# Kernel optimization log

Measured on AMD Instinct MI355X. Metric: run time of the kernel, lower is better.

## Reference

```python
import jax, jax.numpy as jnp
import numpy as np

EPS = 1e-12  # matches torch.nn.functional.normalize eps


def _normalize(v):
    # L2-normalize along last dim, torch-style eps clamp on the norm
    n = jnp.sqrt(jnp.sum(v * v, axis=-1, keepdims=True))
    return v / jnp.maximum(n, EPS)


def _dis_normalized_l2(n1, n2):
    a = _normalize(n1)
    b = _normalize(n2)
    d_minus = jnp.sum((a - b) ** 2, axis=-1)
    d_plus = jnp.sum((a + b) ** 2, axis=-1)
    return jnp.minimum(d_minus, d_plus)


def setup_inputs() -> dict:
    key = jax.random.key(0)
    k1, k2, k3, k4 = jax.random.split(key, 4)
    B, N, M = 8, 4096, 4096
    return {
        "xyz1": jax.random.normal(k1, (B, N, 3), dtype=jnp.float32),
        "xyz2": jax.random.normal(k2, (B, M, 3), dtype=jnp.float32),
        "normal_rebuild": jax.random.normal(k3, (B, N, 3), dtype=jnp.float32),
        "normal_gt": jax.random.normal(k4, (B, M, 3), dtype=jnp.float32),
    }


def reference(xyz1, xyz2, normal_rebuild, normal_gt):
    # Brute-force chamfer: squared pairwise distances [B, N, M]
    sq1 = jnp.sum(xyz1 * xyz1, axis=-1)  # [B, N]
    sq2 = jnp.sum(xyz2 * xyz2, axis=-1)  # [B, M]
    cross = jnp.einsum("bnd,bmd->bnm", xyz1, xyz2)  # [B, N, M]
    D = sq1[:, :, None] + sq2[:, None, :] - 2.0 * cross

    dist1 = jnp.min(D, axis=2)      # [B, N] nearest in xyz2 for each xyz1
    idx1 = jnp.argmin(D, axis=2)    # [B, N]
    dist2 = jnp.min(D, axis=1)      # [B, M]
    idx2 = jnp.argmin(D, axis=1)    # [B, M]

    # Gather matched normals
    target1 = jnp.take_along_axis(normal_gt, idx1[:, :, None], axis=1)       # [B, N, 3]
    target2 = jnp.take_along_axis(normal_rebuild, idx2[:, :, None], axis=1)  # [B, M, 3]

    normal_dist1 = _dis_normalized_l2(normal_rebuild, target1)
    normal_dist2 = _dis_normalized_l2(normal_gt, target2)

    loss_xyz = jnp.mean(dist1) + jnp.mean(dist2)
    loss_normal = jnp.mean(normal_dist1) + jnp.mean(normal_dist2)
    return (loss_xyz, loss_normal)
```

## Files before the change

kernel.cpp:

```cpp
#include <hip/hip_runtime.h>
#include <math.h>

#define NPTS  4096
#define NB    8
#define TPB   1024
#define QB    256
#define HALF  2048
#define SEGS  16
#define CPS   (HALF / SEGS)
#define GRID1 512
#define NQTOT 65536


__global__ __launch_bounds__(TPB, 8) void chamfer5_kernel(
    const float* __restrict__ xyz1, const float* __restrict__ xyz2,
    unsigned long long* __restrict__ res)
{
    __shared__ float4 sc[HALF];
    __shared__ float  sBest[SEGS * QB];
    __shared__ float  qMin[QB];
    __shared__ int    qSeg[QB];
    __shared__ float4 qM[QB];
    __shared__ unsigned long long qPk[QB];

    int bid  = blockIdx.x;
    int dir  = bid >> 8;
    int b    = (bid >> 5) & 7;
    int qblk = (bid >> 1) & 15;
    int half = bid & 1;

    int tid  = threadIdx.x;
    int lane = tid & 63;
    int wid  = tid >> 6;

    const float* qb = (dir ? xyz2 : xyz1) + (size_t)b * NPTS * 3;
    const float* rb = (dir ? xyz1 : xyz2) + ((size_t)b * NPTS + half * HALF) * 3;

    if (tid < 512) {
        const float4* rb4 = (const float4*)rb;
        float4 v0 = rb4[tid * 3 + 0];
        float4 v1 = rb4[tid * 3 + 1];
        float4 v2 = rb4[tid * 3 + 2];
        int p = tid * 4;
        sc[p + 0] = make_float4(v0.x, v0.y, v0.z, fmaf(v0.x, v0.x, fmaf(v0.y, v0.y, v0.z * v0.z)));
        sc[p + 1] = make_float4(v0.w, v1.x, v1.y, fmaf(v0.w, v0.w, fmaf(v1.x, v1.x, v1.y * v1.y)));
        sc[p + 2] = make_float4(v1.z, v1.w, v2.x, fmaf(v1.z, v1.z, fmaf(v1.w, v1.w, v2.x * v2.x)));
        sc[p + 3] = make_float4(v2.y, v2.z, v2.w, fmaf(v2.y, v2.y, fmaf(v2.z, v2.z, v2.w * v2.w)));
    }
    __syncthreads();

    float mx[4], my[4], mz[4];
    #pragma unroll
    for (int u = 0; u < 4; ++u) {
        const float* p = qb + (qblk * QB + u * 64 + lane) * 3;
        mx[u] = -2.f * p[0]; my[u] = -2.f * p[1]; mz[u] = -2.f * p[2];
    }
    float bE[4], bO[4];
    #pragma unroll
    for (int u = 0; u < 4; ++u) { bE[u] = INFINITY; bO[u] = INFINITY; }

    int jb = wid * CPS;
    #pragma unroll 2
    for (int jo = 0; jo < CPS; jo += 4) {
        float4 c0 = sc[jb + jo + 0];
        float4 c1 = sc[jb + jo + 1];
        float4 c2 = sc[jb + jo + 2];
        float4 c3 = sc[jb + jo + 3];
        #pragma unroll
        for (int u = 0; u < 4; ++u) {
            float d0 = fmaf(mx[u], c0.x, fmaf(my[u], c0.y, fmaf(mz[u], c0.z, c0.w)));
            float d1 = fmaf(mx[u], c1.x, fmaf(my[u], c1.y, fmaf(mz[u], c1.z, c1.w)));
            float d2 = fmaf(mx[u], c2.x, fmaf(my[u], c2.y, fmaf(mz[u], c2.z, c2.w)));
            float d3 = fmaf(mx[u], c3.x, fmaf(my[u], c3.y, fmaf(mz[u], c3.z, c3.w)));
            bE[u] = fminf(fminf(bE[u], d0), d2);
            bO[u] = fminf(fminf(bO[u], d1), d3);
        }
    }
    #pragma unroll
    for (int u = 0; u < 4; ++u)
        sBest[wid * QB + u * 64 + lane] = fminf(bE[u], bO[u]);
    __syncthreads();

    if (tid < QB) {
        float best = sBest[tid]; int bs = 0;
        #pragma unroll
        for (int s = 1; s < SEGS; ++s) {
            float v = sBest[s * QB + tid];
            if (v < best) { best = v; bs = s; }
        }
        qMin[tid] = best; qSeg[tid] = bs;
        const float* p = qb + (qblk * QB + tid) * 3;
        float qx = p[0], qy = p[1], qz = p[2];
        qM[tid] = make_float4(-2.f * qx, -2.f * qy, -2.f * qz,
                              fmaf(qx, qx, fmaf(qy, qy, qz * qz)));
    }
    __syncthreads();

    #pragma unroll 4
    for (int k = 0; k < 16; ++k) {
        int q = wid * 16 + k;
        float minv = qMin[q];
        int   seg  = qSeg[q];
        float4 m   = qM[q];
        float4 ca  = sc[seg * CPS + lane];
        float4 cb  = sc[seg * CPS + 64 + lane];
        float da = fmaf(m.x, ca.x, fmaf(m.y, ca.y, fmaf(m.z, ca.z, ca.w)));
        float db = fmaf(m.x, cb.x, fmaf(m.y, cb.y, fmaf(m.z, cb.z, cb.w)));
        unsigned long long ba = __ballot(da == minv);
        unsigned long long bb = __ballot(db == minv);
        if (lane == 0) {
            int off = ba ? (__ffsll(ba) - 1) : (64 + __ffsll(bb) - 1);
            int gidx = half * HALF + seg * CPS + off;
            float dist = fmaxf(minv + m.w, 0.f);
            qPk[q] = ((unsigned long long)__float_as_uint(dist) << 32)
                     | (unsigned)gidx;
        }
    }
    __syncthreads();

    if (tid < QB) {
        unsigned qglob = (unsigned)(dir * (NB * NPTS) + b * NPTS + qblk * QB + tid);
        res[(size_t)half * NQTOT + qglob] = qPk[tid];
    }
}

__global__ __launch_bounds__(TPB) void chamfer5_finalize(
    const float* __restrict__ nrm1, const float* __restrict__ nrm2,
    const unsigned long long* __restrict__ res, float* __restrict__ part)
{
    __shared__ float fin[32];
    int tid = threadIdx.x;
    int gq  = blockIdx.x * TPB + tid;

    unsigned long long pk0 = res[gq];
    unsigned long long pk1 = res[NQTOT + gq];
    unsigned long long pk  = pk0 < pk1 ? pk0 : pk1;
    float dist = __uint_as_float((unsigned)(pk >> 32));
    int   idx  = (int)(pk & 0xFFFFFFFFu);

    int d2  = gq >> 15;
    int rem = gq & 32767;
    int bb  = rem >> 12;

    const float* a3 = (d2 ? nrm2 : nrm1) + (size_t)rem * 3;
    const float* t3 = (d2 ? nrm1 : nrm2) + ((size_t)bb * NPTS + idx) * 3;
    float ax = a3[0], ay = a3[1], az = a3[2];
    float ia = 1.f / fmaxf(sqrtf(fmaf(ax, ax, fmaf(ay, ay, az * az))), 1e-12f);
    ax *= ia; ay *= ia; az *= ia;
    float bx = t3[0], by = t3[1], bz = t3[2];
    float ib = 1.f / fmaxf(sqrtf(fmaf(bx, bx, fmaf(by, by, bz * bz))), 1e-12f);
    bx *= ib; by *= ib; bz *= ib;
    float ex = ax - bx, ey = ay - by, ez = az - bz;
    float px = ax + bx, py = ay + by, pz = az + bz;
    float dm = fmaf(ex, ex, fmaf(ey, ey, ez * ez));
    float dp = fmaf(px, px, fmaf(py, py, pz * pz));
    float nd = fminf(dm, dp);

    for (int off = 32; off > 0; off >>= 1) {
        dist += __shfl_down(dist, off, 64);
        nd   += __shfl_down(nd,   off, 64);
    }
    int wave = tid >> 6, lane = tid & 63;
    if (lane == 0) { fin[wave * 2] = dist; fin[wave * 2 + 1] = nd; }
    __syncthreads();
    if (tid == 0) {
        float a = 0.f, c = 0.f;
        #pragma unroll
        for (int w = 0; w < 16; ++w) { a += fin[w * 2]; c += fin[w * 2 + 1]; }
        part[blockIdx.x * 2 + 0] = a;
        part[blockIdx.x * 2 + 1] = c;
    }
}

__global__ __launch_bounds__(64) void chamfer5_reduce(
    const float* __restrict__ part, float* __restrict__ out)
{
    int t = threadIdx.x;
    float sd = part[t * 2 + 0];
    float sn = part[t * 2 + 1];
    for (int off = 32; off > 0; off >>= 1) {
        sd += __shfl_down(sd, off, 64);
        sn += __shfl_down(sn, off, 64);
    }
    if (t == 0) {
        const float inv = 1.0f / 32768.0f;
        out[0] = sd * inv;
        out[1] = sn * inv;
    }
}

extern "C" void kernel_launch(void* const* d_in, const int* in_sizes, int n_in,
                              void* d_out, int out_size, void* d_ws, size_t ws_size,
                              hipStream_t stream) {
    const float* xyz1 = (const float*)d_in[0];
    const float* xyz2 = (const float*)d_in[1];
    const float* nrm1 = (const float*)d_in[2];
    const float* nrm2 = (const float*)d_in[3];
    float* out = (float*)d_out;

    unsigned long long* res = (unsigned long long*)d_ws;
    float* part = (float*)((char*)d_ws + (size_t)2 * NQTOT * 8);

    chamfer5_kernel<<<GRID1, TPB, 0, stream>>>(xyz1, xyz2, res);
    chamfer5_finalize<<<NQTOT / TPB, TPB, 0, stream>>>(nrm1, nrm2, res, part);
    chamfer5_reduce<<<1, 64, 0, stream>>>(part, out);
}
```

Measured before the change: 88.37 us.

## Retile chamfer scan to 512 queries x 1024-point chunks, fuse reduction via atomics

The scan kernel now gives each block 512 queries against a 1024-point reference chunk, split four ways instead of two, so each thread holds 8 queries in registers and reuses every shared-memory point load across more FMAs. Distances are encoded monotonically so negative values still compare correctly when packed, which replaces the clamp to zero. The separate final reduction kernel is removed. The finalize kernel now uses 256-thread blocks that atomically add scaled partial sums into an output the scan kernel zeroes. This cuts one launch and raises arithmetic intensity, at the cost of more register pressure, four partial results per query, and a float atomic summation order that is not deterministic.

```diff
diff --git a/kernel.cpp b/kernel.cpp
--- a/kernel.cpp
+++ b/kernel.cpp
@@ -1,42 +1,55 @@
 #include <hip/hip_runtime.h>
 #include <math.h>
 
-#define NPTS  4096
-#define NB    8
-#define TPB   1024
-#define QB    256
-#define HALF  2048
-#define SEGS  16
-#define CPS   (HALF / SEGS)
-#define GRID1 512
-#define NQTOT 65536
-
-
-__global__ __launch_bounds__(TPB, 8) void chamfer5_kernel(
+#define NPTS   4096
+#define NB     8
+#define TPB    1024
+#define QB     512
+#define CHUNK  1024
+#define SEGS   16
+#define CPS    (CHUNK / SEGS)
+#define NCHUNK 4
+#define GRID1  512
+#define NQTOT  65536
+
+__device__ __forceinline__ unsigned f2mono(float f) {
+    unsigned b = __float_as_uint(f);
+    unsigned mask = (unsigned)(((int)b) >> 31) | 0x80000000u;
+    return b ^ mask;
+}
+__device__ __forceinline__ float mono2f(unsigned u) {
+    unsigned mask = (u >> 31) ? 0x80000000u : 0xFFFFFFFFu;
+    return __uint_as_float(u ^ mask);
+}
+
+
+__global__ __launch_bounds__(TPB, 8) void chamfer6_scan(
     const float* __restrict__ xyz1, const float* __restrict__ xyz2,
-    unsigned long long* __restrict__ res)
+    unsigned long long* __restrict__ res, float* __restrict__ out)
 {
-    __shared__ float4 sc[HALF];
+    __shared__ float4 sc[CHUNK];
     __shared__ float  sBest[SEGS * QB];
     __shared__ float  qMin[QB];
     __shared__ int    qSeg[QB];
     __shared__ float4 qM[QB];
     __shared__ unsigned long long qPk[QB];
 
-    int bid  = blockIdx.x;
-    int dir  = bid >> 8;
-    int b    = (bid >> 5) & 7;
-    int qblk = (bid >> 1) & 15;
-    int half = bid & 1;
+    int bid   = blockIdx.x;
+    int dir   = bid >> 8;
+    int b     = (bid >> 5) & 7;
+    int qblk  = (bid >> 2) & 7;
+    int chunk = bid & 3;
 
     int tid  = threadIdx.x;
     int lane = tid & 63;
     int wid  = tid >> 6;
 
+    if (bid == 0 && tid == 0) { out[0] = 0.f; out[1] = 0.f; }
+
     const float* qb = (dir ? xyz2 : xyz1) + (size_t)b * NPTS * 3;
-    const float* rb = (dir ? xyz1 : xyz2) + ((size_t)b * NPTS + half * HALF) * 3;
-
-    if (tid < 512) {
+    const float* rb = (dir ? xyz1 : xyz2) + ((size_t)b * NPTS + chunk * CHUNK) * 3;
+
+    if (tid < CHUNK / 4) {
         const float4* rb4 = (const float4*)rb;
         float4 v0 = rb4[tid * 3 + 0];
         float4 v1 = rb4[tid * 3 + 1];
@@ -47,17 +60,21 @@
         sc[p + 2] = make_float4(v1.z, v1.w, v2.x, fmaf(v1.z, v1.z, fmaf(v1.w, v1.w, v2.x * v2.x)));
         sc[p + 3] = make_float4(v2.y, v2.z, v2.w, fmaf(v2.y, v2.y, fmaf(v2.z, v2.z, v2.w * v2.w)));
     }
-    __syncthreads();
-
-    float mx[4], my[4], mz[4];
+    if (tid < QB) {
+        const float* p = qb + (qblk * QB + tid) * 3;
+        float qx = p[0], qy = p[1], qz = p[2];
+        qM[tid] = make_float4(-2.f * qx, -2.f * qy, -2.f * qz,
+                              fmaf(qx, qx, fmaf(qy, qy, qz * qz)));
+    }
+    __syncthreads();
+
+    float mx[8], my[8], mz[8], bE[8];
     #pragma unroll
-    for (int u = 0; u < 4; ++u) {
-        const float* p = qb + (qblk * QB + u * 64 + lane) * 3;
-        mx[u] = -2.f * p[0]; my[u] = -2.f * p[1]; mz[u] = -2.f * p[2];
-    }
-    float bE[4], bO[4];
-    #pragma unroll
-    for (int u = 0; u < 4; ++u) { bE[u] = INFINITY; bO[u] = INFINITY; }
+    for (int u = 0; u < 8; ++u) {
+        float4 m = qM[u * 64 + lane];
+        mx[u] = m.x; my[u] = m.y; mz[u] = m.z;
+        bE[u] = INFINITY;
+    }
 
     int jb = wid * CPS;
     #pragma unroll 2
@@ -67,18 +84,18 @@
         float4 c2 = sc[jb + jo + 2];
         float4 c3 = sc[jb + jo + 3];
         #pragma unroll
-        for (int u = 0; u < 4; ++u) {
+        for (int u = 0; u < 8; ++u) {
             float d0 = fmaf(mx[u], c0.x, fmaf(my[u], c0.y, fmaf(mz[u], c0.z, c0.w)));
             float d1 = fmaf(mx[u], c1.x, fmaf(my[u], c1.y, fmaf(mz[u], c1.z, c1.w)));
             float d2 = fmaf(mx[u], c2.x, fmaf(my[u], c2.y, fmaf(mz[u], c2.z, c2.w)));
             float d3 = fmaf(mx[u], c3.x, fmaf(my[u], c3.y, fmaf(mz[u], c3.z, c3.w)));
-            bE[u] = fminf(fminf(bE[u], d0), d2);
-            bO[u] = fminf(fminf(bO[u], d1), d3);
+            bE[u] = fminf(fminf(bE[u], d0), d1);
+            bE[u] = fminf(fminf(bE[u], d2), d3);
         }
     }
     #pragma unroll
-    for (int u = 0; u < 4; ++u)
-        sBest[wid * QB + u * 64 + lane] = fminf(bE[u], bO[u]);
+    for (int u = 0; u < 8; ++u)
+        sBest[wid * QB + u * 64 + lane] = bE[u];
     __syncthreads();
 
     if (tid < QB) {
@@ -89,53 +106,48 @@
             if (v < best) { best = v; bs = s; }
         }
         qMin[tid] = best; qSeg[tid] = bs;
-        const float* p = qb + (qblk * QB + tid) * 3;
-        float qx = p[0], qy = p[1], qz = p[2];
-        qM[tid] = make_float4(-2.f * qx, -2.f * qy, -2.f * qz,
-                              fmaf(qx, qx, fmaf(qy, qy, qz * qz)));
     }
     __syncthreads();
 
     #pragma unroll 4
-    for (int k = 0; k < 16; ++k) {
-        int q = wid * 16 + k;
+    for (int k = 0; k < QB / SEGS; ++k) {
+        int q = wid * (QB / SEGS) + k;
         float minv = qMin[q];
         int   seg  = qSeg[q];
         float4 m   = qM[q];
         float4 ca  = sc[seg * CPS + lane];
-        float4 cb  = sc[seg * CPS + 64 + lane];
         float da = fmaf(m.x, ca.x, fmaf(m.y, ca.y, fmaf(m.z, ca.z, ca.w)));
-        float db = fmaf(m.x, cb.x, fmaf(m.y, cb.y, fmaf(m.z, cb.z, cb.w)));
         unsigned long long ba = __ballot(da == minv);
-        unsigned long long bb = __ballot(db == minv);
         if (lane == 0) {
-            int off = ba ? (__ffsll(ba) - 1) : (64 + __ffsll(bb) - 1);
-            int gidx = half * HALF + seg * CPS + off;
-            float dist = fmaxf(minv + m.w, 0.f);
-            qPk[q] = ((unsigned long long)__float_as_uint(dist) << 32)
-                     | (unsigned)gidx;
+            int off  = __ffsll(ba) - 1;
+            int gidx = chunk * CHUNK + seg * CPS + off;
+            float dist = minv + m.w;
+            qPk[q] = ((unsigned long long)f2mono(dist) << 32) | (unsigned)gidx;
         }
     }
     __syncthreads();
 
     if (tid < QB) {
         unsigned qglob = (unsigned)(dir * (NB * NPTS) + b * NPTS + qblk * QB + tid);
-        res[(size_t)half * NQTOT + qglob] = qPk[tid];
-    }
-}
-
-__global__ __launch_bounds__(TPB) void chamfer5_finalize(
+        res[(size_t)chunk * NQTOT + qglob] = qPk[tid];
+    }
+}
+
+__global__ __launch_bounds__(256) void chamfer6_finalize(
     const float* __restrict__ nrm1, const float* __restrict__ nrm2,
-    const unsigned long long* __restrict__ res, float* __restrict__ part)
+    const unsigned long long* __restrict__ res, float* __restrict__ out)
 {
-    __shared__ float fin[32];
+    __shared__ float fin[8];
     int tid = threadIdx.x;
-    int gq  = blockIdx.x * TPB + tid;
-
-    unsigned long long pk0 = res[gq];
-    unsigned long long pk1 = res[NQTOT + gq];
-    unsigned long long pk  = pk0 < pk1 ? pk0 : pk1;
-    float dist = __uint_as_float((unsigned)(pk >> 32));
+    int gq  = blockIdx.x * 256 + tid;
+
+    unsigned long long pk = res[gq];
+    #pragma unroll
+    for (int c = 1; c < NCHUNK; ++c) {
+        unsigned long long p2 = res[(size_t)c * NQTOT + gq];
+        pk = p2 < pk ? p2 : pk;
+    }
+    float dist = mono2f((unsigned)(pk >> 32));
     int   idx  = (int)(pk & 0xFFFFFFFFu);
 
     int d2  = gq >> 15;
@@ -164,28 +176,11 @@
     if (lane == 0) { fin[wave * 2] = dist; fin[wave * 2 + 1] = nd; }
     __syncthreads();
     if (tid == 0) {
-        float a = 0.f, c = 0.f;
-        #pragma unroll
-        for (int w = 0; w < 16; ++w) { a += fin[w * 2]; c += fin[w * 2 + 1]; }
-        part[blockIdx.x * 2 + 0] = a;
-        part[blockIdx.x * 2 + 1] = c;
-    }
-}
-
-__global__ __launch_bounds__(64) void chamfer5_reduce(
-    const float* __restrict__ part, float* __restrict__ out)
-{
-    int t = threadIdx.x;
-    float sd = part[t * 2 + 0];
-    float sn = part[t * 2 + 1];
-    for (int off = 32; off > 0; off >>= 1) {
-        sd += __shfl_down(sd, off, 64);
-        sn += __shfl_down(sn, off, 64);
-    }
-    if (t == 0) {
         const float inv = 1.0f / 32768.0f;
-        out[0] = sd * inv;
-        out[1] = sn * inv;
+        float a = (fin[0] + fin[2] + fin[4] + fin[6]) * inv;
+        float c = (fin[1] + fin[3] + fin[5] + fin[7]) * inv;
+        atomicAdd(&out[0], a);
+        atomicAdd(&out[1], c);
     }
 }
 
@@ -199,9 +194,7 @@
     float* out = (float*)d_out;
 
     unsigned long long* res = (unsigned long long*)d_ws;
-    float* part = (float*)((char*)d_ws + (size_t)2 * NQTOT * 8);
-
-    chamfer5_kernel<<<GRID1, TPB, 0, stream>>>(xyz1, xyz2, res);
-    chamfer5_finalize<<<NQTOT / TPB, TPB, 0, stream>>>(nrm1, nrm2, res, part);
-    chamfer5_reduce<<<1, 64, 0, stream>>>(part, out);
-}
+
+    chamfer6_scan<<<GRID1, TPB, 0, stream>>>(xyz1, xyz2, res, out);
+    chamfer6_finalize<<<NQTOT / 256, 256, 0, stream>>>(nrm1, nrm2, res, out);
+}
```

New measurement: 95.63 us. 1.08x slower.
